# Kernel tuning notes

Measured on AMD Instinct MI355X. Metric: run time of the kernel, lower is better.

Reference implementation:

```python
import jax, jax.numpy as jnp
import numpy as np

B, T, D, H, L, V, CTX = 4, 2048, 256, 8, 12, 256, 2048
HD = D // H


def _ln(x, w, b, eps=1e-5):
    m = x.mean(-1, keepdims=True)
    v = ((x - m) ** 2).mean(-1, keepdims=True)
    return (x - m) * jax.lax.rsqrt(v + eps) * w + b


def setup_inputs() -> dict:
    key = jax.random.key(0)
    ks = jax.random.split(key, 16)
    s = 0.02
    inp = {
        "x": jax.random.randint(ks[0], (B, T), 0, V, dtype=jnp.int32),
        "tok_embed": jax.random.normal(ks[1], (V, D), jnp.float32) * s,
        "pos_embed": jax.random.normal(ks[2], (CTX, D), jnp.float32) * s,
        # stacked per-layer params (leading axis = layer)
        "ln1_w": jnp.ones((L, D), jnp.float32),
        "ln1_b": jnp.zeros((L, D), jnp.float32),
        "qkv_w": jax.random.normal(ks[3], (L, D, 3 * D), jnp.float32) * s,
        "qkv_b": jnp.zeros((L, 3 * D), jnp.float32),
        "out_w": jax.random.normal(ks[4], (L, D, D), jnp.float32) * s,
        "out_b": jnp.zeros((L, D), jnp.float32),
        "ln2_w": jnp.ones((L, D), jnp.float32),
        "ln2_b": jnp.zeros((L, D), jnp.float32),
        "fc1_w": jax.random.normal(ks[5], (L, D, 4 * D), jnp.float32) * s,
        "fc1_b": jnp.zeros((L, 4 * D), jnp.float32),
        "fc2_w": jax.random.normal(ks[6], (L, 4 * D, D), jnp.float32) * s,
        "fc2_b": jnp.zeros((L, D), jnp.float32),
        "lnf_w": jnp.ones((D,), jnp.float32),
        "lnf_b": jnp.zeros((D,), jnp.float32),
        "head_w": jax.random.normal(ks[7], (D, V), jnp.float32) * s,
        "head_b": jnp.zeros((V,), jnp.float32),
    }
    return inp


def _forward(x, tok_embed, pos_embed, ln1_w, ln1_b, qkv_w, qkv_b, out_w, out_b,
             ln2_w, ln2_b, fc1_w, fc1_b, fc2_w, fc2_b, lnf_w, lnf_b, head_w, head_b):
    Tcur = x.shape[1]
    h = tok_embed[x] + pos_embed[:Tcur][None, :, :]  # (B,T,D)
    causal = jnp.triu(jnp.ones((Tcur, Tcur), bool), k=1)  # True above diagonal
    scale = jnp.sqrt(jnp.asarray(HD, h.dtype))

    def step(h, p):
        (l1w, l1b, qw, qb, ow, ob, l2w, l2b, f1w, f1b, f2w, f2b) = p
        # attention
        z = _ln(h, l1w, l1b)
        qkv = z @ qw + qb  # (B,T,3D)
        qkv = qkv.reshape(h.shape[0], Tcur, 3, H, HD)
        q, k, v = qkv[:, :, 0], qkv[:, :, 1], qkv[:, :, 2]  # (B,T,H,HD)
        attn = jnp.einsum('bqhd,bkhd->bhqk', q, k) / scale
        attn = jnp.where(causal, -jnp.inf, attn)
        attn = jax.nn.softmax(attn, axis=-1)
        o = jnp.einsum('bhqk,bkhd->bqhd', attn, v).reshape(h.shape[0], Tcur, D)
        h = h + o @ ow + ob
        # MLP (torch nn.GELU default = exact erf gelu)
        z = _ln(h, l2w, l2b)
        z = jax.nn.gelu(z @ f1w + f1b, approximate=False)
        h = h + z @ f2w + f2b
        return h, None

    params = (ln1_w, ln1_b, qkv_w, qkv_b, out_w, out_b,
              ln2_w, ln2_b, fc1_w, fc1_b, fc2_w, fc2_b)
    h, _ = jax.lax.scan(step, h, params)
    h = _ln(h, lnf_w, lnf_b)
    return h @ head_w + head_b  # (B,T,V)


def reference(x, tok_embed, pos_embed, ln1_w, ln1_b, qkv_w, qkv_b, out_w, out_b,
              ln2_w, ln2_b, fc1_w, fc1_b, fc2_w, fc2_b, lnf_w, lnf_b, head_w, head_b):
    return _forward(x, tok_embed, pos_embed, ln1_w, ln1_b, qkv_w, qkv_b, out_w, out_b,
                    ln2_w, ln2_b, fc1_w, fc1_b, fc2_w, fc2_b, lnf_w, lnf_b, head_w, head_b)
```

## Files before the change

### kernel.cpp

```cpp
#include <hip/hip_runtime.h>
#include <cstdint>

#define TT 2048
#define DD 256
#define HH 8
#define LL 12

typedef __attribute__((ext_vector_type(8))) short s16x8;
typedef __attribute__((ext_vector_type(4))) float f32x4;

__device__ __forceinline__ unsigned short f2bf(float f) {
  union { float f; unsigned u; } v; v.f = f;
  return (unsigned short)((v.u + 0x7FFFu + ((v.u >> 16) & 1u)) >> 16);
}

__device__ __forceinline__ float geluf(float x) {
  return 0.5f * x * (1.0f + erff(x * 0.70710678118654752f));
}

__device__ __forceinline__ float fexp2(float x) {
  float r;
  asm("v_exp_f32 %0, %1" : "=v"(r) : "v"(x));
  return r;
}

__device__ __forceinline__ void gload16(const void* g, void* l) {
  __builtin_amdgcn_global_load_lds((const __attribute__((address_space(1))) unsigned int*)g,
                                   (__attribute__((address_space(3))) unsigned int*)l, 16, 0, 0);
}

__global__ __launch_bounds__(256) void k_embed(const int* __restrict__ x,
                                               const float* __restrict__ tok,
                                               const float* __restrict__ pos,
                                               float* __restrict__ h) {
  int i = blockIdx.x * 256 + threadIdx.x;
  int row = i >> 6, c = i & 63;
  int t = x[row];
  f32x4 tv = ((const f32x4*)(tok + (size_t)t * DD))[c];
  f32x4 pv = ((const f32x4*)(pos + (size_t)(row & (TT - 1)) * DD))[c];
  ((f32x4*)(h + (size_t)row * DD))[c] = tv + pv;
}

__global__ __launch_bounds__(256) void k_ln(const float* __restrict__ h,
                                            const float* __restrict__ wgt,
                                            const float* __restrict__ bia,
                                            unsigned short* __restrict__ z) {
  int row = blockIdx.x * 4 + (threadIdx.x >> 6);
  int lane = threadIdx.x & 63;
  f32x4 v = ((const f32x4*)(h + (size_t)row * DD))[lane];
  float s = v[0] + v[1] + v[2] + v[3];
#pragma unroll
  for (int m = 32; m; m >>= 1) s += __shfl_xor(s, m);
  float mean = s * (1.0f / DD);
  f32x4 d = v - mean;
  float s2 = d[0] * d[0] + d[1] * d[1] + d[2] * d[2] + d[3] * d[3];
#pragma unroll
  for (int m = 32; m; m >>= 1) s2 += __shfl_xor(s2, m);
  float inv = rsqrtf(s2 * (1.0f / DD) + 1e-5f);
  f32x4 wv = ((const f32x4*)wgt)[lane];
  f32x4 bv = ((const f32x4*)bia)[lane];
  union { unsigned short us[4]; unsigned long long u64; } ou;
#pragma unroll
  for (int e = 0; e < 4; ++e) ou.us[e] = f2bf(d[e] * inv * wv[e] + bv[e]);
  *(unsigned long long*)(z + (size_t)row * DD + lane * 4) = ou.u64;
}

__global__ __launch_bounds__(256) void k_cast_all(const float* __restrict__ qw, const float* __restrict__ ow,
                                                  const float* __restrict__ f1, const float* __restrict__ f2,
                                                  unsigned short* __restrict__ dst) {
  const int l = blockIdx.y;
  const int t0 = blockIdx.x * 256 + threadIdx.x;
  const int stride = gridDim.x * 256;
  const float* qwl = qw + (size_t)l * 196608;
  const float* owl = ow + (size_t)l * 65536;
  const float* f1l = f1 + (size_t)l * 262144;
  const float* f2l = f2 + (size_t)l * 262144;
  unsigned short* dq = dst + (size_t)l * 786432;
  unsigned short* dO = dq + 196608;
  unsigned short* d1 = dO + 65536;
  unsigned short* d2 = d1 + 262144;
  for (int i = t0; i < 196608; i += stride) dq[i] = f2bf(qwl[(i & 255) * 768 + (i >> 8)]);
  for (int i = t0; i < 65536; i += stride) dO[i] = f2bf(owl[(i & 255) * 256 + (i >> 8)]);
  for (int i = t0; i < 262144; i += stride) d1[i] = f2bf(f1l[(i & 255) * 1024 + (i >> 8)]);
  for (int i = t0; i < 262144; i += stride) d2[i] = f2bf(f2l[(i & 1023) * 256 + (i >> 10)]);
}

__global__ __launch_bounds__(256) void k_cast_tr4(const float* __restrict__ qw, const float* __restrict__ ow,
                                                  const float* __restrict__ f1, const float* __restrict__ f2,
                                                  unsigned short* __restrict__ dq, unsigned short* __restrict__ dO,
                                                  unsigned short* __restrict__ d1, unsigned short* __restrict__ d2) {
  int t0 = blockIdx.x * 256 + threadIdx.x;
  int stride = gridDim.x * 256;
  for (int i = t0; i < 196608; i += stride) dq[i] = f2bf(qw[(i & 255) * 768 + (i >> 8)]);
  for (int i = t0; i < 65536; i += stride) dO[i] = f2bf(ow[(i & 255) * 256 + (i >> 8)]);
  for (int i = t0; i < 262144; i += stride) d1[i] = f2bf(f1[(i & 255) * 1024 + (i >> 8)]);
  for (int i = t0; i < 262144; i += stride) d2[i] = f2bf(f2[(i & 1023) * 256 + (i >> 10)]);
}

__global__ __launch_bounds__(256) void k_cast_tr256(const float* __restrict__ src, unsigned short* __restrict__ dst) {
  int i = blockIdx.x * 256 + threadIdx.x;
  dst[i] = f2bf(src[(i & 255) * 256 + (i >> 8)]);
}

template <int MODE, int MI>
__global__ __launch_bounds__(256, 2) void k_gemm(const unsigned short* __restrict__ A,
                                                 const unsigned short* __restrict__ BT,
                                                 const float* __restrict__ bias,
                                                 void* out, const float* resid,
                                                 int M, int N, int K) {
  __shared__ __align__(16) unsigned short As[2][MI * 32 * 64];
  __shared__ __align__(16) unsigned short Bs[2][128 * 64];
  const int tid = threadIdx.x;
  const int lane = tid & 63, wv = tid >> 6;
  const int wr = wv >> 1, wc = wv & 1;
  const int l15 = lane & 15, g = lane >> 4;
  const int BM = MI * 32;
  const int tm = blockIdx.y, tn = blockIdx.x;
  f32x4 acc[MI][4] = {};
  const int nk = K >> 6;
  const unsigned short* Ag0 = A + (size_t)tm * BM * K;
  const unsigned short* Bg0 = BT + (size_t)tn * 128 * K;
  const int srow = tid >> 3, spart = tid & 7;

#pragma unroll
  for (int it = 0; it < MI; ++it)
    gload16(Ag0 + (size_t)(it * 32 + srow) * K + spart * 8, As[0] + (it * 256 + tid) * 8);
#pragma unroll
  for (int it = 0; it < 4; ++it)
    gload16(Bg0 + (size_t)(it * 32 + srow) * K + spart * 8, Bs[0] + (it * 256 + tid) * 8);
  __syncthreads();

  int buf = 0;
  for (int kt = 0; kt < nk; ++kt) {
    const bool have_next = (kt + 1 < nk);
    if (have_next) {
#pragma unroll
      for (int it = 0; it < MI; ++it)
        gload16(Ag0 + (size_t)(it * 32 + srow) * K + (kt + 1) * 64 + spart * 8,
                As[buf ^ 1] + (it * 256 + tid) * 8);
#pragma unroll
      for (int it = 0; it < 4; ++it)
        gload16(Bg0 + (size_t)(it * 32 + srow) * K + (kt + 1) * 64 + spart * 8,
                Bs[buf ^ 1] + (it * 256 + tid) * 8);
    }
#pragma unroll
    for (int ks = 0; ks < 2; ++ks) {
      s16x8 af[MI], bf[4];
#pragma unroll
      for (int mi = 0; mi < MI; ++mi)
        af[mi] = *(const s16x8*)(As[buf] + (wr * MI * 16 + mi * 16 + l15) * 64 + ks * 32 + g * 8);
#pragma unroll
      for (int ni = 0; ni < 4; ++ni)
        bf[ni] = *(const s16x8*)(Bs[buf] + (wc * 64 + ni * 16 + l15) * 64 + ks * 32 + g * 8);
#pragma unroll
      for (int mi = 0; mi < MI; ++mi)
#pragma unroll
        for (int ni = 0; ni < 4; ++ni)
          acc[mi][ni] = __builtin_amdgcn_mfma_f32_16x16x32_bf16(af[mi], bf[ni], acc[mi][ni], 0, 0, 0);
    }
    if (have_next) {
      __syncthreads();
      buf ^= 1;
    }
  }
#pragma unroll
  for (int ni = 0; ni < 4; ++ni) {
    int col = tn * 128 + wc * 64 + ni * 16 + l15;
    float bv = bias[col];
#pragma unroll
    for (int mi = 0; mi < MI; ++mi) {
      int row0 = tm * BM + wr * MI * 16 + mi * 16 + g * 4;
#pragma unroll
      for (int r = 0; r < 4; ++r) {
        size_t idx = (size_t)(row0 + r) * N + col;
        float vvv = acc[mi][ni][r] + bv;
        if (MODE == 0) ((unsigned short*)out)[idx] = f2bf(vvv);
        else if (MODE == 1) ((unsigned short*)out)[idx] = f2bf(geluf(vvv));
        else if (MODE == 2) ((float*)out)[idx] = resid[idx] + vvv;
        else ((float*)out)[idx] = vvv;
      }
    }
  }
}

__global__ __launch_bounds__(256, 2) void k_attn(const unsigned short* __restrict__ qkv,
                                                 unsigned short* __restrict__ o) {
  __shared__ __align__(16) unsigned short Ks[2][128 * 40];
  __shared__ __align__(16) unsigned short Vs[2][2 * 32 * 72];
  __shared__ __align__(16) unsigned short Ps[4][2 * 16 * 72];
  const int tid = threadIdx.x, lane = tid & 63, w = tid >> 6;
  const int l15 = lane & 15, g = lane >> 4;
  const int p = blockIdx.x;
  const int b = blockIdx.y >> 3, hh = blockIdx.y & 7;
  const size_t base = (size_t)b * TT * 768 + hh * 32;
  const float scl2 = 0.25503492f;
  const int qt0 = p, qt1 = 31 - p;
  const int nt0 = (qt0 >> 1) + 1;
  const int kr = tid >> 1, khf = tid & 1;
  const int vk = tid & 127, vdh = tid >> 7;
  const int vkh = vk >> 6, vklo = vk & 63;
  unsigned short* Pw = &Ps[w][0];

  s16x8 qf0 = *(const s16x8*)(qkv + base + (size_t)(qt0 * 64 + w * 16 + l15) * 768 + g * 8);
  s16x8 qf1 = *(const s16x8*)(qkv + base + (size_t)(qt1 * 64 + w * 16 + l15) * 768 + g * 8);

  {
    const unsigned short* kp = qkv + base + (size_t)kr * 768 + 256 + khf * 16;
    s16x8 k0 = *(const s16x8*)kp;
    s16x8 k1 = *(const s16x8*)(kp + 8);
    const unsigned short* vp = qkv + base + (size_t)vk * 768 + 512 + vdh * 16;
    s16x8 v0 = *(const s16x8*)vp;
    s16x8 v1 = *(const s16x8*)(vp + 8);
    *(s16x8*)(Ks[0] + kr * 40 + khf * 16) = k0;
    *(s16x8*)(Ks[0] + kr * 40 + khf * 16 + 8) = k1;
    unsigned short* vb = Vs[0] + vkh * 2304;
#pragma unroll
    for (int e = 0; e < 8; ++e) {
      int d0 = vdh * 16 + e, d1 = vdh * 16 + 8 + e;
      vb[d0 * 72 + (vklo ^ (((d0 >> 3) & 3) << 4))] = (unsigned short)v0[e];
      vb[d1 * 72 + (vklo ^ (((d1 >> 3) & 3) << 4))] = (unsigned short)v1[e];
    }
  }
  __syncthreads();

  f32x4 accO[2] = {};
  float mM = -3.0e38f, ls = 0.f;

  for (int t = 0; t < 17; ++t) {
    const int buf = t & 1;
    const bool ph = (t >= nt0);
    const int qt = ph ? qt1 : qt0;
    const int j = ph ? t - nt0 : t;
    const bool have_next = (t + 1 < 17);
    s16x8 k0n, k1n, v0n, v1n;
    if (have_next) {
      const int jn = (t + 1 >= nt0) ? t + 1 - nt0 : t + 1;
      const unsigned short* kp = qkv + base + (size_t)(jn * 128 + kr) * 768 + 256 + khf * 16;
      k0n = *(const s16x8*)kp;
      k1n = *(const s16x8*)(kp + 8);
      const unsigned short* vp = qkv + base + (size_t)(jn * 128 + vk) * 768 + 512 + vdh * 16;
      v0n = *(const s16x8*)vp;
      v1n = *(const s16x8*)(vp + 8);
    }
    const int rel = qt * 64 + w * 16 - j * 128;
    const bool full = (rel >= 127);
    int cbm = (rel + 15) >> 4; if (cbm > 7) cbm = 7;
    f32x4 st[8];
#pragma unroll
    for (int cb = 0; cb < 8; ++cb)
      if (cb <= cbm) {
        s16x8 kf = *(const s16x8*)(Ks[buf] + (cb * 16 + l15) * 40 + g * 8);
        f32x4 zz = {};
        st[cb] = __builtin_amdgcn_mfma_f32_16x16x32_bf16(kf, ph ? qf1 : qf0, zz, 0, 0, 0);
      }
    float rmax = -3.0e38f;
#pragma unroll
    for (int cb = 0; cb < 8; ++cb)
      if (cb <= cbm) {
#pragma unroll
        for (int r = 0; r < 4; ++r) {
          float s = st[cb][r] * scl2;
          if (!full && (cb * 16 + g * 4 + r) > rel + l15) s = -3.0e38f;
          st[cb][r] = s;
          rmax = fmaxf(rmax, s);
        }
      }
    rmax = fmaxf(rmax, __shfl_xor(rmax, 16));
    rmax = fmaxf(rmax, __shfl_xor(rmax, 32));
    float al = 1.0f;
    if (!__all(rmax <= mM + 11.5f)) {
      float nm = fmaxf(mM, rmax);
      al = fexp2(mM - nm);
      mM = nm;
#pragma unroll
      for (int r = 0; r < 4; ++r) {
        float aw = __shfl(al, g * 4 + r);
        accO[0][r] *= aw;
        accO[1][r] *= aw;
      }
    }
    float rsum = 0.f;
#pragma unroll
    for (int cb = 0; cb < 8; ++cb)
      if (cb <= cbm) {
        union { unsigned short us[4]; unsigned long long u; } pk;
#pragma unroll
        for (int r = 0; r < 4; ++r) {
          float pe = fexp2(st[cb][r] - mM);
          rsum += pe;
          pk.us[r] = f2bf(pe);
        }
        *(unsigned long long*)(Pw + (cb >> 2) * 1152 + l15 * 72 + (cb & 3) * 16 + g * 4) = pk.u;
      }
    if (cbm < 7 && !(cbm & 1))
      *(unsigned long long*)(Pw + ((cbm + 1) >> 2) * 1152 + l15 * 72 + ((cbm + 1) & 3) * 16 + g * 4) = 0ULL;
    rsum += __shfl_xor(rsum, 16);
    rsum += __shfl_xor(rsum, 32);
    ls = ls * al + rsum;
    asm volatile("s_waitcnt lgkmcnt(0)" ::: "memory");
    __builtin_amdgcn_sched_barrier(0);
    const int kcm = cbm >> 1;
#pragma unroll
    for (int kc = 0; kc < 4; ++kc)
      if (kc <= kcm) {
        s16x8 pa = *(const s16x8*)(Pw + (kc >> 1) * 1152 + l15 * 72 + (kc & 1) * 32 + g * 8);
        s16x8 bv0, bv1;
#pragma unroll
        for (int hb = 0; hb < 2; ++hb) {
          const int d = hb * 16 + l15;
          const int kxr = ((kc & 1) * 32 + g * 8) ^ (((d >> 3) & 3) << 4);
          if (hb == 0) bv0 = *(const s16x8*)(Vs[buf] + (kc >> 1) * 2304 + d * 72 + kxr);
          else bv1 = *(const s16x8*)(Vs[buf] + (kc >> 1) * 2304 + d * 72 + kxr);
        }
        accO[0] = __builtin_amdgcn_mfma_f32_16x16x32_bf16(pa, bv0, accO[0], 0, 0, 0);
        accO[1] = __builtin_amdgcn_mfma_f32_16x16x32_bf16(pa, bv1, accO[1], 0, 0, 0);
      }
    if (have_next) {
      *(s16x8*)(Ks[buf ^ 1] + kr * 40 + khf * 16) = k0n;
      *(s16x8*)(Ks[buf ^ 1] + kr * 40 + khf * 16 + 8) = k1n;
      unsigned short* vb = Vs[buf ^ 1] + vkh * 2304;
#pragma unroll
      for (int e = 0; e < 8; ++e) {
        int d0 = vdh * 16 + e, d1 = vdh * 16 + 8 + e;
        vb[d0 * 72 + (vklo ^ (((d0 >> 3) & 3) << 4))] = (unsigned short)v0n[e];
        vb[d1 * 72 + (vklo ^ (((d1 >> 3) & 3) << 4))] = (unsigned short)v1n[e];
      }
      __syncthreads();
    }
    if (t == nt0 - 1) {
      float inv = 1.0f / ls;
#pragma unroll
      for (int r = 0; r < 4; ++r) {
        float lv = __shfl(inv, g * 4 + r);
        int row = qt0 * 64 + w * 16 + g * 4 + r;
        o[(size_t)(b * TT + row) * DD + hh * 32 + l15] = f2bf(accO[0][r] * lv);
        o[(size_t)(b * TT + row) * DD + hh * 32 + 16 + l15] = f2bf(accO[1][r] * lv);
      }
      accO[0] = f32x4{};
      accO[1] = f32x4{};
      mM = -3.0e38f;
      ls = 0.f;
    }
  }
  {
    float inv = 1.0f / ls;
#pragma unroll
    for (int r = 0; r < 4; ++r) {
      float lv = __shfl(inv, g * 4 + r);
      int row = qt1 * 64 + w * 16 + g * 4 + r;
      o[(size_t)(b * TT + row) * DD + hh * 32 + l15] = f2bf(accO[0][r] * lv);
      o[(size_t)(b * TT + row) * DD + hh * 32 + 16 + l15] = f2bf(accO[1][r] * lv);
    }
  }
}

extern "C" void kernel_launch(void* const* d_in, const int* in_sizes, int n_in,
                              void* d_out, int out_size, void* d_ws, size_t ws_size,
                              hipStream_t stream) {
  const int* x = (const int*)d_in[0];
  const float* tok = (const float*)d_in[1];
  const float* pos = (const float*)d_in[2];
  const float* ln1w = (const float*)d_in[3];
  const float* ln1b = (const float*)d_in[4];
  const float* qkvw = (const float*)d_in[5];
  const float* qkvb = (const float*)d_in[6];
  const float* outw = (const float*)d_in[7];
  const float* outb = (const float*)d_in[8];
  const float* ln2w = (const float*)d_in[9];
  const float* ln2b = (const float*)d_in[10];
  const float* f1w = (const float*)d_in[11];
  const float* f1b = (const float*)d_in[12];
  const float* f2w = (const float*)d_in[13];
  const float* f2b = (const float*)d_in[14];
  const float* lnfw = (const float*)d_in[15];
  const float* lnfb = (const float*)d_in[16];
  const float* hw = (const float*)d_in[17];
  const float* hb = (const float*)d_in[18];

  char* ws = (char*)d_ws;
  float* h = (float*)(ws + 0);
  unsigned short* z = (unsigned short*)(ws + 8388608);
  unsigned short* qkvB = (unsigned short*)(ws + 12582912);
  unsigned short* ob = (unsigned short*)(ws + 25165824);
  unsigned short* a1 = (unsigned short*)(ws + 29360128);
  unsigned short* wAll = (unsigned short*)(ws + 46137344);
  const bool bigws = ws_size >= 65142784ULL;
  unsigned short* wh = (unsigned short*)(ws + (bigws ? 65011712 : 47710208));

  if (bigws)
    k_cast_all<<<dim3(256, 12), dim3(256), 0, stream>>>(qkvw, outw, f1w, f2w, wAll);
  k_cast_tr256<<<dim3(256), dim3(256), 0, stream>>>(hw, wh);
  k_embed<<<dim3(2048), dim3(256), 0, stream>>>(x, tok, pos, h);

  for (int l = 0; l < LL; ++l) {
    unsigned short* wq = wAll + (size_t)(bigws ? l : 0) * 786432;
    unsigned short* wo = wq + 196608;
    unsigned short* w1 = wo + 65536;
    unsigned short* w2 = w1 + 262144;
    if (!bigws)
      k_cast_tr4<<<dim3(1024), dim3(256), 0, stream>>>(
          qkvw + (size_t)l * 196608, outw + (size_t)l * 65536,
          f1w + (size_t)l * 262144, f2w + (size_t)l * 262144, wq, wo, w1, w2);
    k_ln<<<dim3(2048), dim3(256), 0, stream>>>(h, ln1w + l * 256, ln1b + l * 256, z);
    k_gemm<0, 4><<<dim3(6, 64), dim3(256), 0, stream>>>(z, wq, qkvb + l * 768, qkvB, nullptr, 8192, 768, 256);
    k_attn<<<dim3(16, 32), dim3(256), 0, stream>>>(qkvB, ob);
    k_gemm<2, 2><<<dim3(2, 128), dim3(256), 0, stream>>>(ob, wo, outb + l * 256, h, h, 8192, 256, 256);
    k_ln<<<dim3(2048), dim3(256), 0, stream>>>(h, ln2w + l * 256, ln2b + l * 256, z);
    k_gemm<1, 4><<<dim3(8, 64), dim3(256), 0, stream>>>(z, w1, f1b + l * 1024, a1, nullptr, 8192, 1024, 256);
    k_gemm<2, 2><<<dim3(2, 128), dim3(256), 0, stream>>>(a1, w2, f2b + l * 256, h, h, 8192, 256, 1024);
  }

  k_ln<<<dim3(2048), dim3(256), 0, stream>>>(h, lnfw, lnfb, z);
  k_gemm<3, 2><<<dim3(2, 128), dim3(256), 0, stream>>>(z, wh, hb, d_out, nullptr, 8192, 256, 256);
}
```

Baseline: 1.551 ms.

## Tile weight transpose via LDS, use packed bf16 converts, fold softmax scale

```diff
diff --git a/kernel.cpp b/kernel.cpp
--- a/kernel.cpp
+++ b/kernel.cpp
@@ -12,6 +12,12 @@
 __device__ __forceinline__ unsigned short f2bf(float f) {
   union { float f; unsigned u; } v; v.f = f;
   return (unsigned short)((v.u + 0x7FFFu + ((v.u >> 16) & 1u)) >> 16);
+}
+
+__device__ __forceinline__ unsigned cvtpk(float lo, float hi) {
+  unsigned r;
+  asm("v_cvt_pk_bf16_f32 %0, %1, %2" : "=v"(r) : "v"(lo), "v"(hi));
+  return r;
 }
 
 __device__ __forceinline__ float geluf(float x) {
@@ -59,30 +65,50 @@
   float inv = rsqrtf(s2 * (1.0f / DD) + 1e-5f);
   f32x4 wv = ((const f32x4*)wgt)[lane];
   f32x4 bv = ((const f32x4*)bia)[lane];
-  union { unsigned short us[4]; unsigned long long u64; } ou;
-#pragma unroll
-  for (int e = 0; e < 4; ++e) ou.us[e] = f2bf(d[e] * inv * wv[e] + bv[e]);
-  *(unsigned long long*)(z + (size_t)row * DD + lane * 4) = ou.u64;
+  float o0 = d[0] * inv * wv[0] + bv[0], o1 = d[1] * inv * wv[1] + bv[1];
+  float o2 = d[2] * inv * wv[2] + bv[2], o3 = d[3] * inv * wv[3] + bv[3];
+  unsigned long long u64 = (unsigned long long)cvtpk(o0, o1) |
+                           ((unsigned long long)cvtpk(o2, o3) << 32);
+  *(unsigned long long*)(z + (size_t)row * DD + lane * 4) = u64;
 }
 
 __global__ __launch_bounds__(256) void k_cast_all(const float* __restrict__ qw, const float* __restrict__ ow,
                                                   const float* __restrict__ f1, const float* __restrict__ f2,
                                                   unsigned short* __restrict__ dst) {
+  __shared__ float Tt[32][33];
   const int l = blockIdx.y;
-  const int t0 = blockIdx.x * 256 + threadIdx.x;
-  const int stride = gridDim.x * 256;
-  const float* qwl = qw + (size_t)l * 196608;
-  const float* owl = ow + (size_t)l * 65536;
-  const float* f1l = f1 + (size_t)l * 262144;
-  const float* f2l = f2 + (size_t)l * 262144;
-  unsigned short* dq = dst + (size_t)l * 786432;
-  unsigned short* dO = dq + 196608;
-  unsigned short* d1 = dO + 65536;
-  unsigned short* d2 = d1 + 262144;
-  for (int i = t0; i < 196608; i += stride) dq[i] = f2bf(qwl[(i & 255) * 768 + (i >> 8)]);
-  for (int i = t0; i < 65536; i += stride) dO[i] = f2bf(owl[(i & 255) * 256 + (i >> 8)]);
-  for (int i = t0; i < 262144; i += stride) d1[i] = f2bf(f1l[(i & 255) * 1024 + (i >> 8)]);
-  for (int i = t0; i < 262144; i += stride) d2[i] = f2bf(f2l[(i & 1023) * 256 + (i >> 10)]);
+  const int t = blockIdx.x;
+  const float* src;
+  unsigned short* d;
+  int K, N, tk, tn;
+  if (t < 192) {
+    src = qw + (size_t)l * 196608; d = dst + (size_t)l * 786432;
+    K = 256; N = 768; tk = t / 24; tn = t % 24;
+  } else if (t < 256) {
+    int t2 = t - 192;
+    src = ow + (size_t)l * 65536; d = dst + (size_t)l * 786432 + 196608;
+    K = 256; N = 256; tk = t2 >> 3; tn = t2 & 7;
+  } else if (t < 512) {
+    int t3 = t - 256;
+    src = f1 + (size_t)l * 262144; d = dst + (size_t)l * 786432 + 262144;
+    K = 256; N = 1024; tk = t3 >> 5; tn = t3 & 31;
+  } else {
+    int t4 = t - 512;
+    src = f2 + (size_t)l * 262144; d = dst + (size_t)l * 786432 + 524288;
+    K = 1024; N = 256; tk = t4 >> 3; tn = t4 & 7;
+  }
+  const int tx = threadIdx.x & 31, ty = threadIdx.x >> 5;
+#pragma unroll
+  for (int r = 0; r < 4; ++r) {
+    int row = ty + r * 8;
+    Tt[row][tx] = src[(size_t)(tk * 32 + row) * N + tn * 32 + tx];
+  }
+  __syncthreads();
+#pragma unroll
+  for (int r = 0; r < 4; ++r) {
+    int row = ty + r * 8;
+    d[(size_t)(tn * 32 + row) * K + tk * 32 + tx] = f2bf(Tt[tx][row]);
+  }
 }
 
 __global__ __launch_bounds__(256) void k_cast_tr4(const float* __restrict__ qw, const float* __restrict__ ow,
@@ -257,19 +283,20 @@
 #pragma unroll
     for (int cb = 0; cb < 8; ++cb)
       if (cb <= cbm) {
-#pragma unroll
-        for (int r = 0; r < 4; ++r) {
-          float s = st[cb][r] * scl2;
-          if (!full && (cb * 16 + g * 4 + r) > rel + l15) s = -3.0e38f;
-          st[cb][r] = s;
-          rmax = fmaxf(rmax, s);
+        if (!full) {
+#pragma unroll
+          for (int r = 0; r < 4; ++r)
+            if ((cb * 16 + g * 4 + r) > rel + l15) st[cb][r] = -3.0e38f;
         }
+#pragma unroll
+        for (int r = 0; r < 4; ++r) rmax = fmaxf(rmax, st[cb][r]);
       }
     rmax = fmaxf(rmax, __shfl_xor(rmax, 16));
     rmax = fmaxf(rmax, __shfl_xor(rmax, 32));
+    const float rs = rmax * scl2;
     float al = 1.0f;
-    if (!__all(rmax <= mM + 11.5f)) {
-      float nm = fmaxf(mM, rmax);
+    if (!__all(rs <= mM + 11.5f)) {
+      float nm = fmaxf(mM, rs);
       al = fexp2(mM - nm);
       mM = nm;
 #pragma unroll
@@ -283,14 +310,14 @@
 #pragma unroll
     for (int cb = 0; cb < 8; ++cb)
       if (cb <= cbm) {
-        union { unsigned short us[4]; unsigned long long u; } pk;
-#pragma unroll
-        for (int r = 0; r < 4; ++r) {
-          float pe = fexp2(st[cb][r] - mM);
-          rsum += pe;
-          pk.us[r] = f2bf(pe);
-        }
-        *(unsigned long long*)(Pw + (cb >> 2) * 1152 + l15 * 72 + (cb & 3) * 16 + g * 4) = pk.u;
+        float p0 = fexp2(fmaf(st[cb][0], scl2, -mM));
+        float p1 = fexp2(fmaf(st[cb][1], scl2, -mM));
+        float p2 = fexp2(fmaf(st[cb][2], scl2, -mM));
+        float p3 = fexp2(fmaf(st[cb][3], scl2, -mM));
+        rsum += (p0 + p1) + (p2 + p3);
+        unsigned long long u = (unsigned long long)cvtpk(p0, p1) |
+                               ((unsigned long long)cvtpk(p2, p3) << 32);
+        *(unsigned long long*)(Pw + (cb >> 2) * 1152 + l15 * 72 + (cb & 3) * 16 + g * 4) = u;
       }
     if (cbm < 7 && !(cbm & 1))
       *(unsigned long long*)(Pw + ((cbm + 1) >> 2) * 1152 + l15 * 72 + ((cbm + 1) & 3) * 16 + g * 4) = 0ULL;
@@ -388,7 +415,7 @@
   unsigned short* wh = (unsigned short*)(ws + (bigws ? 65011712 : 47710208));
 
   if (bigws)
-    k_cast_all<<<dim3(256, 12), dim3(256), 0, stream>>>(qkvw, outw, f1w, f2w, wAll);
+    k_cast_all<<<dim3(768, 12), dim3(256), 0, stream>>>(qkvw, outw, f1w, f2w, wAll);
   k_cast_tr256<<<dim3(256), dim3(256), 0, stream>>>(hw, wh);
   k_embed<<<dim3(2048), dim3(256), 0, stream>>>(x, tok, pos, h);
 
```

Measured after the change: 1.529 ms. Within noise of the previous version (-1.4%).
